# Optimization experiments

Measured on AMD Instinct MI355X. Metric: run time of the kernel, lower is better.

Reference implementation:

```python
import jax, jax.numpy as jnp
import numpy as np

POOL = 7
IMG = 1024.0
NUM_CLASSES = 2
R = 1000


def crop_and_resize(feat, boxes, pool):
    # feat: [C,H,W]; boxes: [N,4] normalized (y1,x1,y2,x2); returns [N,C,pool,pool]
    C, H, W = feat.shape
    y1, x1, y2, x2 = boxes[:, 0], boxes[:, 1], boxes[:, 2], boxes[:, 3]
    t = jnp.arange(pool, dtype=feat.dtype) / (pool - 1)
    ys = (y1[:, None] + (y2 - y1)[:, None] * t[None, :]) * (H - 1)  # [N,P]
    xs = (x1[:, None] + (x2 - x1)[:, None] * t[None, :]) * (W - 1)  # [N,P]
    vy = (ys >= 0) & (ys <= H - 1)
    vx = (xs >= 0) & (xs <= W - 1)
    yf = jnp.floor(ys)
    xf = jnp.floor(xs)
    wy = (ys - yf)[None, :, :, None]  # [1,N,P,1]
    wx = (xs - xf)[None, :, None, :]  # [1,N,1,P]
    y0 = jnp.clip(yf, 0, H - 1).astype(jnp.int32)
    y1i = jnp.clip(yf + 1, 0, H - 1).astype(jnp.int32)
    x0 = jnp.clip(xf, 0, W - 1).astype(jnp.int32)
    x1i = jnp.clip(xf + 1, 0, W - 1).astype(jnp.int32)

    def g(yi, xi):  # gather -> [C,N,P,P]
        return feat[:, yi[:, :, None], xi[:, None, :]]

    val = (g(y0, x0) * (1 - wy) * (1 - wx)
           + g(y0, x1i) * (1 - wy) * wx
           + g(y1i, x0) * wy * (1 - wx)
           + g(y1i, x1i) * wy * wx)
    mask = (vy[:, :, None] & vx[:, None, :])[None]  # extrapolation value 0
    return jnp.where(mask, val, 0.0).transpose(1, 0, 2, 3)


def roi_align(feats, rois_flat):
    # rois_flat: [N,4] in pixel coords (x1,y1,x2,y2)
    x1, y1, x2, y2 = rois_flat[:, 0], rois_flat[:, 1], rois_flat[:, 2], rois_flat[:, 3]
    lvl = jnp.log2(jnp.sqrt((y2 - y1) * (x2 - x1)) / 224.0)
    lvl = jnp.clip(jnp.round(lvl) + 4, 2, 5)
    boxes = rois_flat[:, jnp.array([1, 0, 3, 2])] / IMG  # (y1,x1,y2,x2) normalized
    crops = jnp.stack([crop_and_resize(f[0], boxes, POOL) for f in feats])  # [4,N,C,P,P]
    sel = (lvl[None, :] == jnp.arange(2, 6, dtype=lvl.dtype)[:, None])       # [4,N]
    return jnp.sum(jnp.where(sel[:, :, None, None, None], crops, 0.0), axis=0)  # [N,C,P,P]


def setup_inputs() -> dict:
    key = jax.random.key(0)
    ks = jax.random.split(key, 24)
    feat2 = jax.random.normal(ks[0], (1, 256, 256, 256), jnp.float32)
    feat3 = jax.random.normal(ks[1], (1, 256, 128, 128), jnp.float32)
    feat4 = jax.random.normal(ks[2], (1, 256, 64, 64), jnp.float32)
    feat5 = jax.random.normal(ks[3], (1, 256, 32, 32), jnp.float32)
    x1 = jax.random.uniform(ks[4], (1, R), minval=0.0, maxval=900.0)
    y1 = jax.random.uniform(ks[5], (1, R), minval=0.0, maxval=900.0)
    w = jax.random.uniform(ks[6], (1, R), minval=16.0, maxval=400.0)
    h = jax.random.uniform(ks[7], (1, R), minval=16.0, maxval=400.0)
    rois = jnp.stack([x1, y1, jnp.minimum(x1 + w, 1023.0), jnp.minimum(y1 + h, 1023.0)], axis=-1)
    s = 0.02
    params = dict(
        conv_w=s * jax.random.normal(ks[8], (1024, 256, POOL, POOL), jnp.float32),
        conv_b=jnp.zeros((1024,), jnp.float32),
        bn_gamma=jnp.ones((1024,), jnp.float32),
        bn_beta=jnp.zeros((1024,), jnp.float32),
        bn_mean=jnp.zeros((1024,), jnp.float32),
        bn_var=jnp.ones((1024,), jnp.float32),
        fc1_w=s * jax.random.normal(ks[9], (1024, 1024), jnp.float32),
        fc1_b=jnp.zeros((1024,), jnp.float32),
        fc2_w=s * jax.random.normal(ks[10], (1024, 1024), jnp.float32),
        fc2_b=jnp.zeros((1024,), jnp.float32),
        cls_w=s * jax.random.normal(ks[11], (NUM_CLASSES, 1024), jnp.float32),
        cls_b=jnp.zeros((NUM_CLASSES,), jnp.float32),
        bbox_w=s * jax.random.normal(ks[12], (NUM_CLASSES * 4, 1024), jnp.float32),
        bbox_b=jnp.zeros((NUM_CLASSES * 4,), jnp.float32),
    )
    return dict(feat2=feat2, feat3=feat3, feat4=feat4, feat5=feat5, rois=rois, **params)


def reference(feat2, feat3, feat4, feat5, rois, conv_w, conv_b, bn_gamma, bn_beta,
              bn_mean, bn_var, fc1_w, fc1_b, fc2_w, fc2_b, cls_w, cls_b, bbox_w, bbox_b):
    roi_number = rois.shape[1]
    pooled = roi_align([feat2, feat3, feat4, feat5], rois.reshape(-1, 4))  # [N,256,7,7]
    # conv1 (7x7 valid on 7x7 input -> 1x1 spatial) + BN (inference stats, eps=1e-3)
    y = jnp.einsum('nchw,ochw->no', pooled, conv_w) + conv_b
    y = (y - bn_mean) / jnp.sqrt(bn_var + 1e-3) * bn_gamma + bn_beta
    h = jax.nn.relu(y @ fc1_w.T + fc1_b)
    h = jax.nn.relu(h @ fc2_w.T + fc2_b)
    logits = h @ cls_w.T + cls_b
    probs = jax.nn.softmax(logits, axis=-1)
    bbox = h @ bbox_w.T + bbox_b
    return (logits.reshape(1, roi_number, NUM_CLASSES),
            probs.reshape(1, roi_number, NUM_CLASSES),
            bbox.reshape(1, roi_number, NUM_CLASSES, 4))
```

## Files before the change

kernel.cpp:

```cpp
#include <hip/hip_runtime.h>
#include <cstdint>
#include <cstddef>

typedef __attribute__((ext_vector_type(8))) short bf16x8;
typedef __attribute__((ext_vector_type(4))) float f32x4;

#define POOLK 12544

#define TOFF2 0
#define TOFF3 16777216
#define TOFF4 20971520
#define TOFF5 22020096
#define TTOT_SH 22282240

__device__ __forceinline__ void gld16(const void* g, void* l) {
    __builtin_amdgcn_global_load_lds(
        (const __attribute__((address_space(1))) void*)g,
        (__attribute__((address_space(3))) void*)l, 16, 0, 0);
}

__device__ __forceinline__ unsigned short f32_to_bf16(float f) {
    union { float f; unsigned u; } x; x.f = f;
    unsigned r = (x.u + 0x7FFFu + ((x.u >> 16) & 1u)) >> 16;
    return (unsigned short)r;
}
__device__ __forceinline__ float bf16_to_f32(unsigned short s) {
    return __uint_as_float(((unsigned)s) << 16);
}

__global__ __launch_bounds__(256) void feat_tr_kernel(
    const float* __restrict__ f2, const float* __restrict__ f3,
    const float* __restrict__ f4, const float* __restrict__ f5,
    unsigned short* __restrict__ T)
{
    int b = blockIdx.x;
    const float* src; unsigned short* dst; int P;
    if (b < 2048)      { src = f2; dst = T + TOFF2; P = 65536; }
    else if (b < 2560) { src = f3; dst = T + TOFF3; P = 16384; b -= 2048; }
    else if (b < 2688) { src = f4; dst = T + TOFF4; P = 4096;  b -= 2560; }
    else               { src = f5; dst = T + TOFF5; P = 1024;  b -= 2688; }
    const int p0 = b * 32;
    __shared__ float lds[32][260];
    const int t = threadIdx.x;
    const int cr = t >> 3, x4 = (t & 7) * 4;
#pragma unroll
    for (int cc = 0; cc < 8; ++cc) {
        const int c = cc * 32 + cr;
        const float4 v = *(const float4*)(src + (size_t)c * P + p0 + x4);
        lds[x4+0][c] = v.x; lds[x4+1][c] = v.y;
        lds[x4+2][c] = v.z; lds[x4+3][c] = v.w;
    }
    __syncthreads();
    const int c0 = (t & 31) * 8;
#pragma unroll
    for (int pz = 0; pz < 4; ++pz) {
        const int pp = pz * 8 + (t >> 5);
        const float4 a = *(const float4*)&lds[pp][c0];
        const float4 bq = *(const float4*)&lds[pp][c0 + 4];
        bf16x8 o;
        o[0] = (short)f32_to_bf16(a.x);  o[1] = (short)f32_to_bf16(a.y);
        o[2] = (short)f32_to_bf16(a.z);  o[3] = (short)f32_to_bf16(a.w);
        o[4] = (short)f32_to_bf16(bq.x); o[5] = (short)f32_to_bf16(bq.y);
        o[6] = (short)f32_to_bf16(bq.z); o[7] = (short)f32_to_bf16(bq.w);
        *(bf16x8*)(dst + ((size_t)(p0 + pp)) * 256 + c0) = o;
    }
}

__global__ __launch_bounds__(256) void roi_gather_kernel(
    const unsigned short* __restrict__ T, const float* __restrict__ rois,
    unsigned short* __restrict__ pooled)
{
    const int n = blockIdx.x;
    const int tid = threadIdx.x;
    __shared__ int sy0[7], sy1[7], sx0[7], sx1[7];
    __shared__ float swy[7], swx[7], svy[7], svx[7];

    const float rx1 = rois[n*4+0], ry1 = rois[n*4+1];
    const float rx2 = rois[n*4+2], ry2 = rois[n*4+3];
    int lvl = (int)rintf(log2f(sqrtf((ry2-ry1)*(rx2-rx1)) * (1.0f/224.0f))) + 4;
    lvl = lvl < 2 ? 2 : (lvl > 5 ? 5 : lvl);
    const int W = 256 >> (lvl - 2);
    const float Hm1 = (float)(W - 1);
    const unsigned short* Tl = T + (lvl == 2 ? TOFF2 : (lvl == 3 ? TOFF3 : (lvl == 4 ? TOFF4 : TOFF5)));

    if (tid < 7) {
        const float t = (float)tid / 6.0f;
        const float by1 = ry1*(1.0f/1024.0f), by2 = ry2*(1.0f/1024.0f);
        const float bx1 = rx1*(1.0f/1024.0f), bx2 = rx2*(1.0f/1024.0f);
        const float ys = (by1 + (by2 - by1) * t) * Hm1;
        const float xs = (bx1 + (bx2 - bx1) * t) * Hm1;
        const float yf = floorf(ys), xf = floorf(xs);
        swy[tid] = ys - yf;  swx[tid] = xs - xf;
        sy0[tid] = (int)fminf(fmaxf(yf,        0.0f), Hm1);
        sy1[tid] = (int)fminf(fmaxf(yf + 1.0f, 0.0f), Hm1);
        sx0[tid] = (int)fminf(fmaxf(xf,        0.0f), Hm1);
        sx1[tid] = (int)fminf(fmaxf(xf + 1.0f, 0.0f), Hm1);
        svy[tid] = (ys >= 0.0f && ys <= Hm1) ? 1.0f : 0.0f;
        svx[tid] = (xs >= 0.0f && xs <= Hm1) ? 1.0f : 0.0f;
    }
    __syncthreads();

    const int g  = tid >> 5;
    const int c0 = (tid & 31) * 8;
    unsigned short* orow = pooled + (size_t)n * POOLK;
#pragma unroll
    for (int it = 0; it < 7; ++it) {
        const int pos = it * 8 + g;
        if (pos >= 49) break;
        const int i = pos / 7, j = pos % 7;
        const int y0 = sy0[i], y1 = sy1[i], x0 = sx0[j], x1 = sx1[j];
        const float wy = swy[i], wx = swx[j];
        const float scale = svy[i] * svx[j];
        const bf16x8 v00 = *(const bf16x8*)(Tl + ((size_t)(y0*W + x0))*256 + c0);
        const bf16x8 v01 = *(const bf16x8*)(Tl + ((size_t)(y0*W + x1))*256 + c0);
        const bf16x8 v10 = *(const bf16x8*)(Tl + ((size_t)(y1*W + x0))*256 + c0);
        const bf16x8 v11 = *(const bf16x8*)(Tl + ((size_t)(y1*W + x1))*256 + c0);
        bf16x8 o;
#pragma unroll
        for (int jj = 0; jj < 8; ++jj) {
            const float f00 = bf16_to_f32((unsigned short)v00[jj]);
            const float f01 = bf16_to_f32((unsigned short)v01[jj]);
            const float f10 = bf16_to_f32((unsigned short)v10[jj]);
            const float f11 = bf16_to_f32((unsigned short)v11[jj]);
            const float top = f00 + (f01 - f00) * wx;
            const float bot = f10 + (f11 - f10) * wx;
            o[jj] = (short)f32_to_bf16((top + (bot - top) * wy) * scale);
        }
        *(bf16x8*)(orow + pos * 256 + c0) = o;
    }
}

__global__ __launch_bounds__(256) void roi_direct_kernel(
    const float* __restrict__ feat2, const float* __restrict__ feat3,
    const float* __restrict__ feat4, const float* __restrict__ feat5,
    const float* __restrict__ rois, unsigned short* __restrict__ pooled)
{
    const int n = blockIdx.x;
    const int tid = threadIdx.x;
    __shared__ int sy0[7], sy1[7], sx0[7], sx1[7];
    __shared__ float swy[7], swx[7], svy[7], svx[7];
    const float rx1 = rois[n*4+0], ry1 = rois[n*4+1];
    const float rx2 = rois[n*4+2], ry2 = rois[n*4+3];
    int lvl = (int)rintf(log2f(sqrtf((ry2-ry1)*(rx2-rx1)) * (1.0f/224.0f))) + 4;
    lvl = lvl < 2 ? 2 : (lvl > 5 ? 5 : lvl);
    const int H = 256 >> (lvl - 2);
    const float Hm1 = (float)(H - 1);
    const float* feat = lvl==2 ? feat2 : (lvl==3 ? feat3 : (lvl==4 ? feat4 : feat5));
    if (tid < 7) {
        const float t = (float)tid / 6.0f;
        const float by1 = ry1*(1.0f/1024.0f), by2 = ry2*(1.0f/1024.0f);
        const float bx1 = rx1*(1.0f/1024.0f), bx2 = rx2*(1.0f/1024.0f);
        const float ys = (by1 + (by2-by1)*t) * Hm1;
        const float xs = (bx1 + (bx2-bx1)*t) * Hm1;
        const float yf = floorf(ys), xf = floorf(xs);
        swy[tid] = ys - yf;  swx[tid] = xs - xf;
        sy0[tid] = (int)fminf(fmaxf(yf,      0.0f), Hm1);
        sy1[tid] = (int)fminf(fmaxf(yf+1.0f, 0.0f), Hm1);
        sx0[tid] = (int)fminf(fmaxf(xf,      0.0f), Hm1);
        sx1[tid] = (int)fminf(fmaxf(xf+1.0f, 0.0f), Hm1);
        svy[tid] = (ys >= 0.0f && ys <= Hm1) ? 1.0f : 0.0f;
        svx[tid] = (xs >= 0.0f && xs <= Hm1) ? 1.0f : 0.0f;
    }
    __syncthreads();
    const int HW = H * H;
    unsigned short* orow = pooled + (size_t)n * POOLK;
    for (int e = tid; e < POOLK; e += 256) {
        const int c = e / 49, ij = e % 49, i = ij / 7, j = ij % 7;
        const float* p = feat + c * HW;
        const int y0 = sy0[i], y1 = sy1[i], x0 = sx0[j], x1 = sx1[j];
        const float wy = swy[i], wx = swx[j];
        const float v00 = p[y0*H + x0], v01 = p[y0*H + x1];
        const float v10 = p[y1*H + x0], v11 = p[y1*H + x1];
        float v = v00*(1.0f-wy)*(1.0f-wx) + v01*(1.0f-wy)*wx
                + v10*wy*(1.0f-wx)        + v11*wy*wx;
        v *= svy[i] * svx[j];
        orow[ij*256 + c] = f32_to_bf16(v);
    }
}

__global__ void cvt_bf16_kernel(const float* __restrict__ src,
                                unsigned short* __restrict__ dst, int n)
{
    const int i = (blockIdx.x * 256 + threadIdx.x) * 4;
    if (i >= n) return;
    const float4 v = *(const float4*)(src + i);
    ushort4 o;
    o.x = f32_to_bf16(v.x); o.y = f32_to_bf16(v.y);
    o.z = f32_to_bf16(v.z); o.w = f32_to_bf16(v.w);
    *(ushort4*)(dst + i) = o;
}

__global__ __launch_bounds__(256) void convw_tr_kernel(
    const float* __restrict__ src, unsigned short* __restrict__ dst)
{
    const int o = blockIdx.x;
    const int t = threadIdx.x;
    __shared__ unsigned short wlds[POOLK];
    const float* srow = src + (size_t)o * POOLK;
    for (int it = 0; it < 49; ++it) {
        const int idx = it * 256 + t;
        wlds[idx] = f32_to_bf16(srow[idx]);
    }
    __syncthreads();
    unsigned short* drow = dst + (size_t)o * POOLK;
    for (int it = 0; it < 49; ++it) {
        const int k = it * 256 + t;
        const int c = k & 255, ij = k >> 8;
        drow[k] = wlds[c * 49 + ij];
    }
}

__global__ __launch_bounds__(256, 2) void gemm_bt(
    const unsigned short* __restrict__ A, const unsigned short* __restrict__ B,
    float* __restrict__ Cpart, int K, int Kper, int nz)
{
    __shared__ __align__(16) unsigned short At[128*64];
    __shared__ __align__(16) unsigned short Bt[128*64];
    const int tid  = threadIdx.x;
    const int lane = tid & 63;
    const int bid  = blockIdx.x;
    const int z  = bid % nz;
    const int iq = bid / nz;
    const int bx = iq & 7, by = iq >> 3;
    const int wm = (tid >> 6) >> 1, wn = (tid >> 6) & 1;
    const size_t k0 = (size_t)z * Kper;

    const int r1 = tid >> 3;
    const int q  = tid & 7;
    const int csw = (q ^ (r1 & 7)) * 8;
    const unsigned short* Ag = A + ((size_t)(by * 128 + r1)) * K + k0 + csw;
    const unsigned short* Bg = B + ((size_t)(bx * 128 + r1)) * K + k0 + csw;

    f32x4 acc[4][4] = {};
    const int fr = lane & 15;
    const int fq = lane >> 4;
    const int sA = fr & 7;

    for (int k = 0; k < Kper; k += 64) {
#pragma unroll
        for (int p = 0; p < 4; ++p) {
            gld16(Ag + (size_t)(32 * p) * K + k, &At[p * 2048 + tid * 8]);
            gld16(Bg + (size_t)(32 * p) * K + k, &Bt[p * 2048 + tid * 8]);
        }
        asm volatile("s_waitcnt vmcnt(0)" ::: "memory");
        __syncthreads();

        bf16x8 a[4][2], b[4][2];
#pragma unroll
        for (int mi = 0; mi < 4; ++mi) {
            const int row = wm * 64 + mi * 16 + fr;
#pragma unroll
            for (int kk = 0; kk < 2; ++kk)
                a[mi][kk] = *(const bf16x8*)&At[row * 64 + ((kk * 4 + fq) ^ sA) * 8];
        }
#pragma unroll
        for (int ni = 0; ni < 4; ++ni) {
            const int row = wn * 64 + ni * 16 + fr;
#pragma unroll
            for (int kk = 0; kk < 2; ++kk)
                b[ni][kk] = *(const bf16x8*)&Bt[row * 64 + ((kk * 4 + fq) ^ sA) * 8];
        }
#pragma unroll
        for (int mi = 0; mi < 4; ++mi)
#pragma unroll
            for (int ni = 0; ni < 4; ++ni)
                acc[mi][ni] = __builtin_amdgcn_mfma_f32_16x16x32_bf16(
                    a[mi][0], b[ni][0], acc[mi][ni], 0, 0, 0);
        if (k + 32 < Kper) {
#pragma unroll
            for (int mi = 0; mi < 4; ++mi)
#pragma unroll
                for (int ni = 0; ni < 4; ++ni)
                    acc[mi][ni] = __builtin_amdgcn_mfma_f32_16x16x32_bf16(
                        a[mi][1], b[ni][1], acc[mi][ni], 0, 0, 0);
        }
        __syncthreads();
    }

    float* Cp = Cpart + (size_t)z * (1024 * 1024);
    const int row0 = by * 128 + wm * 64;
    const int col0 = bx * 128 + wn * 64;
#pragma unroll
    for (int mi = 0; mi < 4; ++mi)
#pragma unroll
        for (int ni = 0; ni < 4; ++ni)
#pragma unroll
            for (int r = 0; r < 4; ++r)
                Cp[(size_t)(row0 + mi*16 + fq*4 + r) * 1024 + col0 + ni*16 + fr]
                    = acc[mi][ni][r];
}

__global__ void reduce_bn_kernel(const float* __restrict__ part,
    const float* __restrict__ bias, const float* __restrict__ gamma,
    const float* __restrict__ beta, const float* __restrict__ mean,
    const float* __restrict__ var, unsigned short* __restrict__ out, int nz)
{
    const int i4 = (blockIdx.x * 256 + threadIdx.x) * 4;
    const int n = i4 & 1023;
    float4 v = make_float4(0.f, 0.f, 0.f, 0.f);
    for (int zz = 0; zz < nz; ++zz) {
        const float4 p = *(const float4*)(part + (size_t)zz * 1048576 + i4);
        v.x += p.x; v.y += p.y; v.z += p.z; v.w += p.w;
    }
    const float4 bi = *(const float4*)(bias + n);
    const float4 ga = *(const float4*)(gamma + n);
    const float4 be = *(const float4*)(beta + n);
    const float4 me = *(const float4*)(mean + n);
    const float4 va = *(const float4*)(var + n);
    ushort4 o;
    o.x = f32_to_bf16((v.x + bi.x - me.x) * __frsqrt_rn(va.x + 0.001f) * ga.x + be.x);
    o.y = f32_to_bf16((v.y + bi.y - me.y) * __frsqrt_rn(va.y + 0.001f) * ga.y + be.y);
    o.z = f32_to_bf16((v.z + bi.z - me.z) * __frsqrt_rn(va.z + 0.001f) * ga.z + be.z);
    o.w = f32_to_bf16((v.w + bi.w - me.w) * __frsqrt_rn(va.w + 0.001f) * ga.w + be.w);
    *(ushort4*)(out + i4) = o;
}

__global__ __launch_bounds__(256) void gemm64_fused(
    const unsigned short* __restrict__ A, const unsigned short* __restrict__ B,
    const float* __restrict__ bias, unsigned short* __restrict__ out, int relu)
{
    __shared__ __align__(16) unsigned short At[64*64];
    __shared__ __align__(16) unsigned short Bt[64*64];
    const int tid = threadIdx.x, lane = tid & 63;
    const int w = tid >> 6, wm = w >> 1, wn = w & 1;
    const int r1 = tid >> 3;
    const int q  = tid & 7;
    const int csw = (q ^ (r1 & 7)) * 8;
    const unsigned short* Ag = A + (size_t)(blockIdx.y*64 + r1) * 1024 + csw;
    const unsigned short* Bg = B + (size_t)(blockIdx.x*64 + r1) * 1024 + csw;
    const int fr = lane & 15, fq = lane >> 4;
    const int sA = fr & 7;
    f32x4 acc[2][2] = {};
    for (int k = 0; k < 1024; k += 64) {
#pragma unroll
        for (int p = 0; p < 2; ++p) {
            gld16(Ag + (size_t)(32 * p) * 1024 + k, &At[p * 2048 + tid * 8]);
            gld16(Bg + (size_t)(32 * p) * 1024 + k, &Bt[p * 2048 + tid * 8]);
        }
        asm volatile("s_waitcnt vmcnt(0)" ::: "memory");
        __syncthreads();
        bf16x8 a[2][2], b[2][2];
#pragma unroll
        for (int mi = 0; mi < 2; ++mi) {
            const int row = wm * 32 + mi * 16 + fr;
#pragma unroll
            for (int kk = 0; kk < 2; ++kk)
                a[mi][kk] = *(const bf16x8*)&At[row * 64 + ((kk * 4 + fq) ^ sA) * 8];
        }
#pragma unroll
        for (int ni = 0; ni < 2; ++ni) {
            const int row = wn * 32 + ni * 16 + fr;
#pragma unroll
            for (int kk = 0; kk < 2; ++kk)
                b[ni][kk] = *(const bf16x8*)&Bt[row * 64 + ((kk * 4 + fq) ^ sA) * 8];
        }
#pragma unroll
        for (int kk = 0; kk < 2; ++kk)
#pragma unroll
            for (int mi = 0; mi < 2; ++mi)
#pragma unroll
                for (int ni = 0; ni < 2; ++ni)
                    acc[mi][ni] = __builtin_amdgcn_mfma_f32_16x16x32_bf16(
                        a[mi][kk], b[ni][kk], acc[mi][ni], 0, 0, 0);
        __syncthreads();
    }
    const int row0 = blockIdx.y*64 + wm*32;
    const int col0 = blockIdx.x*64 + wn*32;
#pragma unroll
    for (int mi = 0; mi < 2; ++mi)
#pragma unroll
        for (int ni = 0; ni < 2; ++ni)
#pragma unroll
            for (int r = 0; r < 4; ++r) {
                const int row = row0 + mi*16 + fq*4 + r;
                const int col = col0 + ni*16 + fr;
                float v = acc[mi][ni][r] + bias[col];
                if (relu) v = fmaxf(v, 0.0f);
                out[(size_t)row * 1024 + col] = f32_to_bf16(v);
            }
}

__global__ __launch_bounds__(256) void head_kernel(
    const unsigned short* __restrict__ h2,
    const float* __restrict__ cls_w, const float* __restrict__ cls_b,
    const float* __restrict__ bbox_w, const float* __restrict__ bbox_b,
    float* __restrict__ out)
{
    const int roi = blockIdx.x * 4 + (threadIdx.x >> 6);
    const int lane = threadIdx.x & 63;
    const unsigned short* hrow = h2 + (size_t)roi * 1024;
    float hv[16];
#pragma unroll
    for (int j = 0; j < 16; ++j)
        hv[j] = bf16_to_f32(hrow[lane*16 + j]);
    float r[10];
#pragma unroll
    for (int o = 0; o < 10; ++o) {
        const float* w = (o < 2) ? (cls_w + o*1024) : (bbox_w + (size_t)(o-2)*1024);
        float s = 0.f;
#pragma unroll
        for (int j = 0; j < 16; ++j) s += hv[j] * w[lane*16 + j];
#pragma unroll
        for (int off = 32; off > 0; off >>= 1) s += __shfl_xor(s, off);
        r[o] = s;
    }
    if (lane == 0) {
        const float l0 = r[0] + cls_b[0], l1 = r[1] + cls_b[1];
        out[roi*2+0] = l0; out[roi*2+1] = l1;
        const float m = fmaxf(l0, l1);
        const float e0 = expf(l0 - m), e1 = expf(l1 - m);
        const float inv = 1.0f / (e0 + e1);
        out[2000 + roi*2 + 0] = e0 * inv;
        out[2000 + roi*2 + 1] = e1 * inv;
#pragma unroll
        for (int qq = 0; qq < 8; ++qq) out[4000 + roi*8 + qq] = r[2+qq] + bbox_b[qq];
    }
}

extern "C" void kernel_launch(void* const* d_in, const int* in_sizes, int n_in,
                              void* d_out, int out_size, void* d_ws, size_t ws_size,
                              hipStream_t stream)
{
    const float* feat2   = (const float*)d_in[0];
    const float* feat3   = (const float*)d_in[1];
    const float* feat4   = (const float*)d_in[2];
    const float* feat5   = (const float*)d_in[3];
    const float* rois    = (const float*)d_in[4];
    const float* conv_w  = (const float*)d_in[5];
    const float* conv_b  = (const float*)d_in[6];
    const float* bn_gamma= (const float*)d_in[7];
    const float* bn_beta = (const float*)d_in[8];
    const float* bn_mean = (const float*)d_in[9];
    const float* bn_var  = (const float*)d_in[10];
    const float* fc1_w   = (const float*)d_in[11];
    const float* fc1_b   = (const float*)d_in[12];
    const float* fc2_w   = (const float*)d_in[13];
    const float* fc2_b   = (const float*)d_in[14];
    const float* cls_w   = (const float*)d_in[15];
    const float* cls_b   = (const float*)d_in[16];
    const float* bbox_w  = (const float*)d_in[17];
    const float* bbox_b  = (const float*)d_in[18];
    float* out = (float*)d_out;

    const size_t fixedBytes = (size_t)25690112 + 25690112 + 5 * (size_t)2097152;
    const size_t needA = fixedBytes + (size_t)44564480;
    const size_t needB = fixedBytes + (size_t)16777216;
    int tier = (ws_size >= needA) ? 1 : 2;
    (void)needB;
    const size_t regionA = tier == 1 ? (size_t)44564480 : (size_t)16777216;
    const int nzc  = tier == 1 ? 8 : 4;
    const int Kper = tier == 1 ? 1568 : 3136;

    char* ws = (char*)d_ws;
    size_t off = 0;
    auto alloc = [&](size_t bytes) {
        void* p = ws + off; off += (bytes + 255) & ~(size_t)255; return p;
    };
    char* rA = (char*)alloc(regionA);
    unsigned short* T    = (unsigned short*)rA;
    float*          part = (float*)rA;
    unsigned short* pooled   = (unsigned short*)alloc((size_t)1024 * POOLK * 2);
    unsigned short* convw_bf = (unsigned short*)alloc((size_t)1024 * POOLK * 2);
    unsigned short* fc1w_bf  = (unsigned short*)alloc((size_t)1048576 * 2);
    unsigned short* fc2w_bf  = (unsigned short*)alloc((size_t)1048576 * 2);
    unsigned short* ybf      = (unsigned short*)alloc((size_t)1048576 * 2);
    unsigned short* h1bf     = (unsigned short*)alloc((size_t)1048576 * 2);
    unsigned short* h2bf     = (unsigned short*)alloc((size_t)1048576 * 2);

    hipLaunchKernelGGL(cvt_bf16_kernel, dim3(1024), dim3(256), 0, stream,
                       fc1_w, fc1w_bf, 1048576);
    hipLaunchKernelGGL(cvt_bf16_kernel, dim3(1024), dim3(256), 0, stream,
                       fc2_w, fc2w_bf, 1048576);
    hipLaunchKernelGGL(convw_tr_kernel, dim3(1024), dim3(256), 0, stream,
                       conv_w, convw_bf);

    hipMemsetAsync(pooled + (size_t)1000 * POOLK, 0, (size_t)24 * POOLK * 2, stream);

    if (tier == 1) {
        hipLaunchKernelGGL(feat_tr_kernel, dim3(2720), dim3(256), 0, stream,
                           feat2, feat3, feat4, feat5, T);
        hipLaunchKernelGGL(roi_gather_kernel, dim3(1000), dim3(256), 0, stream,
                           T, rois, pooled);
    } else {
        hipLaunchKernelGGL(roi_direct_kernel, dim3(1000), dim3(256), 0, stream,
                           feat2, feat3, feat4, feat5, rois, pooled);
    }

    hipLaunchKernelGGL(gemm_bt, dim3(64 * nzc), dim3(256), 0, stream,
                       pooled, convw_bf, part, POOLK, Kper, nzc);
    hipLaunchKernelGGL(reduce_bn_kernel, dim3(1024), dim3(256), 0, stream,
                       part, conv_b, bn_gamma, bn_beta, bn_mean, bn_var, ybf, nzc);

    hipLaunchKernelGGL(gemm64_fused, dim3(16, 16), dim3(256), 0, stream,
                       ybf, fc1w_bf, fc1_b, h1bf, 1);
    hipLaunchKernelGGL(gemm64_fused, dim3(16, 16), dim3(256), 0, stream,
                       h1bf, fc2w_bf, fc2_b, h2bf, 1);

    hipLaunchKernelGGL(head_kernel, dim3(250), dim3(256), 0, stream,
                       h2bf, cls_w, cls_b, bbox_w, bbox_b, out);
}
```

Baseline: 132.7 us.

## Fuse prep kernels, fold padding memset into ROI gather, double-buffer GEMM K loops

Merges feature transpose, conv weight transpose and FC weight conversion into one prep launch, now with bf16 LDS staging and XOR swizzle. The padding-row memset moves into the ROI gather kernel. Both GEMMs switch from a single 64-wide K tile to double-buffered 32-wide K tiles that prefetch the next tile while MFMAs run, and raise wave priority around the MFMAs. The goal is fewer launches and less load latency exposed in the GEMM loops, at the cost of more barriers per K step.

```diff
diff --git a/kernel.cpp b/kernel.cpp
--- a/kernel.cpp
+++ b/kernel.cpp
@@ -11,67 +11,103 @@
 #define TOFF3 16777216
 #define TOFF4 20971520
 #define TOFF5 22020096
-#define TTOT_SH 22282240
 
 __device__ __forceinline__ void gld16(const void* g, void* l) {
     __builtin_amdgcn_global_load_lds(
         (const __attribute__((address_space(1))) void*)g,
         (__attribute__((address_space(3))) void*)l, 16, 0, 0);
 }
-
 __device__ __forceinline__ unsigned short f32_to_bf16(float f) {
     union { float f; unsigned u; } x; x.f = f;
-    unsigned r = (x.u + 0x7FFFu + ((x.u >> 16) & 1u)) >> 16;
-    return (unsigned short)r;
+    return (unsigned short)((x.u + 0x7FFFu + ((x.u >> 16) & 1u)) >> 16);
 }
 __device__ __forceinline__ float bf16_to_f32(unsigned short s) {
     return __uint_as_float(((unsigned)s) << 16);
 }
 
-__global__ __launch_bounds__(256) void feat_tr_kernel(
+__global__ __launch_bounds__(256) void prep_kernel(
     const float* __restrict__ f2, const float* __restrict__ f3,
     const float* __restrict__ f4, const float* __restrict__ f5,
-    unsigned short* __restrict__ T)
-{
+    unsigned short* __restrict__ T,
+    const float* __restrict__ conv_w, unsigned short* __restrict__ convw_bf,
+    const float* __restrict__ fc1_w, unsigned short* __restrict__ fc1w_bf,
+    const float* __restrict__ fc2_w, unsigned short* __restrict__ fc2w_bf,
+    int do_feat)
+{
+    __shared__ __align__(16) unsigned short sh[8192];
+    const int t = threadIdx.x;
     int b = blockIdx.x;
-    const float* src; unsigned short* dst; int P;
-    if (b < 2048)      { src = f2; dst = T + TOFF2; P = 65536; }
-    else if (b < 2560) { src = f3; dst = T + TOFF3; P = 16384; b -= 2048; }
-    else if (b < 2688) { src = f4; dst = T + TOFF4; P = 4096;  b -= 2560; }
-    else               { src = f5; dst = T + TOFF5; P = 1024;  b -= 2688; }
-    const int p0 = b * 32;
-    __shared__ float lds[32][260];
-    const int t = threadIdx.x;
-    const int cr = t >> 3, x4 = (t & 7) * 4;
-#pragma unroll
-    for (int cc = 0; cc < 8; ++cc) {
-        const int c = cc * 32 + cr;
-        const float4 v = *(const float4*)(src + (size_t)c * P + p0 + x4);
-        lds[x4+0][c] = v.x; lds[x4+1][c] = v.y;
-        lds[x4+2][c] = v.z; lds[x4+3][c] = v.w;
-    }
-    __syncthreads();
-    const int c0 = (t & 31) * 8;
-#pragma unroll
-    for (int pz = 0; pz < 4; ++pz) {
-        const int pp = pz * 8 + (t >> 5);
-        const float4 a = *(const float4*)&lds[pp][c0];
-        const float4 bq = *(const float4*)&lds[pp][c0 + 4];
-        bf16x8 o;
-        o[0] = (short)f32_to_bf16(a.x);  o[1] = (short)f32_to_bf16(a.y);
-        o[2] = (short)f32_to_bf16(a.z);  o[3] = (short)f32_to_bf16(a.w);
-        o[4] = (short)f32_to_bf16(bq.x); o[5] = (short)f32_to_bf16(bq.y);
-        o[6] = (short)f32_to_bf16(bq.z); o[7] = (short)f32_to_bf16(bq.w);
-        *(bf16x8*)(dst + ((size_t)(p0 + pp)) * 256 + c0) = o;
+
+    if (b < 2720) {
+        if (!do_feat) return;
+        const float* src; unsigned short* dst; int P;
+        if (b < 2048)      { src = f2; dst = T + TOFF2; P = 65536; }
+        else if (b < 2560) { src = f3; dst = T + TOFF3; P = 16384; b -= 2048; }
+        else if (b < 2688) { src = f4; dst = T + TOFF4; P = 4096;  b -= 2560; }
+        else               { src = f5; dst = T + TOFF5; P = 1024;  b -= 2688; }
+        const int p0 = b * 32;
+        const int cr = t >> 3, x4 = (t & 7) * 4;
+#pragma unroll
+        for (int cc = 0; cc < 8; ++cc) {
+            const int c = cc * 32 + cr;
+            const float4 v = *(const float4*)(src + (size_t)c * P + p0 + x4);
+            const int blk = c >> 3, cl = c & 7;
+            float vv[4] = {v.x, v.y, v.z, v.w};
+#pragma unroll
+            for (int i = 0; i < 4; ++i) {
+                const int p = x4 + i;
+                sh[p * 256 + ((blk ^ (p >> 2)) << 3) + cl] = f32_to_bf16(vv[i]);
+            }
+        }
+        __syncthreads();
+        const int cb = t & 31;
+#pragma unroll
+        for (int pz = 0; pz < 4; ++pz) {
+            const int pp = pz * 8 + (t >> 5);
+            const bf16x8 v = *(const bf16x8*)&sh[pp * 256 + ((cb ^ (pp >> 2)) << 3)];
+            *(bf16x8*)(dst + (size_t)(p0 + pp) * 256 + cb * 8) = v;
+        }
+        return;
+    }
+    b -= 2720;
+    if (b < 2048) {
+        const int o = b >> 1, half = b & 1;
+        const float* srow = conv_w + (size_t)o * POOLK + half * 6272;
+        for (int k = t; k < 6272; k += 256) sh[k] = f32_to_bf16(srow[k]);
+        __syncthreads();
+        unsigned short* drow = convw_bf + (size_t)o * POOLK + half * 128;
+        for (int k = t; k < 6272; k += 256) {
+            const int ij = k >> 7, cl = k & 127;
+            drow[ij * 256 + cl] = sh[cl * 49 + ij];
+        }
+        return;
+    }
+    b -= 2048;
+    {
+        const float* src = (b < 1024) ? fc1_w : fc2_w;
+        unsigned short* dst = (b < 1024) ? fc1w_bf : fc2w_bf;
+        const int bb = b & 1023;
+        const int i = (bb * 256 + t) * 4;
+        const float4 v = *(const float4*)(src + i);
+        ushort4 o;
+        o.x = f32_to_bf16(v.x); o.y = f32_to_bf16(v.y);
+        o.z = f32_to_bf16(v.z); o.w = f32_to_bf16(v.w);
+        *(ushort4*)(dst + i) = o;
     }
 }
 
 __global__ __launch_bounds__(256) void roi_gather_kernel(
     const unsigned short* __restrict__ T, const float* __restrict__ rois,
-    unsigned short* __restrict__ pooled)
+    unsigned short* __restrict__ pooled, int nroi)
 {
     const int n = blockIdx.x;
     const int tid = threadIdx.x;
+    unsigned short* orow = pooled + (size_t)n * POOLK;
+    if (n >= nroi) {
+        const bf16x8 z = {};
+        for (int k = tid * 8; k < POOLK; k += 2048) *(bf16x8*)(orow + k) = z;
+        return;
+    }
     __shared__ int sy0[7], sy1[7], sx0[7], sx1[7];
     __shared__ float swy[7], swx[7], svy[7], svx[7];
 
@@ -102,7 +138,6 @@
 
     const int g  = tid >> 5;
     const int c0 = (tid & 31) * 8;
-    unsigned short* orow = pooled + (size_t)n * POOLK;
 #pragma unroll
     for (int it = 0; it < 7; ++it) {
         const int pos = it * 8 + g;
@@ -133,10 +168,16 @@
 __global__ __launch_bounds__(256) void roi_direct_kernel(
     const float* __restrict__ feat2, const float* __restrict__ feat3,
     const float* __restrict__ feat4, const float* __restrict__ feat5,
-    const float* __restrict__ rois, unsigned short* __restrict__ pooled)
+    const float* __restrict__ rois, unsigned short* __restrict__ pooled, int nroi)
 {
     const int n = blockIdx.x;
     const int tid = threadIdx.x;
+    unsigned short* orow = pooled + (size_t)n * POOLK;
+    if (n >= nroi) {
+        const bf16x8 z = {};
+        for (int k = tid * 8; k < POOLK; k += 2048) *(bf16x8*)(orow + k) = z;
+        return;
+    }
     __shared__ int sy0[7], sy1[7], sx0[7], sx1[7];
     __shared__ float swy[7], swx[7], svy[7], svx[7];
     const float rx1 = rois[n*4+0], ry1 = rois[n*4+1];
@@ -163,7 +204,6 @@
     }
     __syncthreads();
     const int HW = H * H;
-    unsigned short* orow = pooled + (size_t)n * POOLK;
     for (int e = tid; e < POOLK; e += 256) {
         const int c = e / 49, ij = e % 49, i = ij / 7, j = ij % 7;
         const float* p = feat + c * HW;
@@ -178,44 +218,12 @@
     }
 }
 
-__global__ void cvt_bf16_kernel(const float* __restrict__ src,
-                                unsigned short* __restrict__ dst, int n)
-{
-    const int i = (blockIdx.x * 256 + threadIdx.x) * 4;
-    if (i >= n) return;
-    const float4 v = *(const float4*)(src + i);
-    ushort4 o;
-    o.x = f32_to_bf16(v.x); o.y = f32_to_bf16(v.y);
-    o.z = f32_to_bf16(v.z); o.w = f32_to_bf16(v.w);
-    *(ushort4*)(dst + i) = o;
-}
-
-__global__ __launch_bounds__(256) void convw_tr_kernel(
-    const float* __restrict__ src, unsigned short* __restrict__ dst)
-{
-    const int o = blockIdx.x;
-    const int t = threadIdx.x;
-    __shared__ unsigned short wlds[POOLK];
-    const float* srow = src + (size_t)o * POOLK;
-    for (int it = 0; it < 49; ++it) {
-        const int idx = it * 256 + t;
-        wlds[idx] = f32_to_bf16(srow[idx]);
-    }
-    __syncthreads();
-    unsigned short* drow = dst + (size_t)o * POOLK;
-    for (int it = 0; it < 49; ++it) {
-        const int k = it * 256 + t;
-        const int c = k & 255, ij = k >> 8;
-        drow[k] = wlds[c * 49 + ij];
-    }
-}
-
 __global__ __launch_bounds__(256, 2) void gemm_bt(
     const unsigned short* __restrict__ A, const unsigned short* __restrict__ B,
     float* __restrict__ Cpart, int K, int Kper, int nz)
 {
-    __shared__ __align__(16) unsigned short At[128*64];
-    __shared__ __align__(16) unsigned short Bt[128*64];
+    __shared__ __align__(16) unsigned short At[2][128*32];
+    __shared__ __align__(16) unsigned short Bt[2][128*32];
     const int tid  = threadIdx.x;
     const int lane = tid & 63;
     const int bid  = blockIdx.x;
@@ -225,56 +233,54 @@
     const int wm = (tid >> 6) >> 1, wn = (tid >> 6) & 1;
     const size_t k0 = (size_t)z * Kper;
 
-    const int r1 = tid >> 3;
-    const int q  = tid & 7;
-    const int csw = (q ^ (r1 & 7)) * 8;
+    const int r1 = tid >> 2;
+    const int q  = tid & 3;
+    const int csw = (q ^ (r1 & 3)) * 8;
     const unsigned short* Ag = A + ((size_t)(by * 128 + r1)) * K + k0 + csw;
     const unsigned short* Bg = B + ((size_t)(bx * 128 + r1)) * K + k0 + csw;
+    const int nit = Kper >> 5;
+
+    gld16(Ag,                  &At[0][tid * 8]);
+    gld16(Ag + (size_t)64 * K, &At[0][(tid + 256) * 8]);
+    gld16(Bg,                  &Bt[0][tid * 8]);
+    gld16(Bg + (size_t)64 * K, &Bt[0][(tid + 256) * 8]);
 
     f32x4 acc[4][4] = {};
     const int fr = lane & 15;
     const int fq = lane >> 4;
-    const int sA = fr & 7;
-
-    for (int k = 0; k < Kper; k += 64) {
-#pragma unroll
-        for (int p = 0; p < 4; ++p) {
-            gld16(Ag + (size_t)(32 * p) * K + k, &At[p * 2048 + tid * 8]);
-            gld16(Bg + (size_t)(32 * p) * K + k, &Bt[p * 2048 + tid * 8]);
+    const int rslot = (fq ^ (fr & 3)) * 8;
+
+    int buf = 0;
+    for (int it = 0; it < nit; ++it) {
+        if (it + 1 < nit) {
+            const size_t ko = (size_t)(it + 1) * 32;
+            gld16(Ag + ko,                  &At[buf ^ 1][tid * 8]);
+            gld16(Ag + (size_t)64 * K + ko, &At[buf ^ 1][(tid + 256) * 8]);
+            gld16(Bg + ko,                  &Bt[buf ^ 1][tid * 8]);
+            gld16(Bg + (size_t)64 * K + ko, &Bt[buf ^ 1][(tid + 256) * 8]);
+            asm volatile("s_waitcnt vmcnt(4)" ::: "memory");
+        } else {
+            asm volatile("s_waitcnt vmcnt(0)" ::: "memory");
         }
-        asm volatile("s_waitcnt vmcnt(0)" ::: "memory");
         __syncthreads();
 
-        bf16x8 a[4][2], b[4][2];
-#pragma unroll
-        for (int mi = 0; mi < 4; ++mi) {
-            const int row = wm * 64 + mi * 16 + fr;
-#pragma unroll
-            for (int kk = 0; kk < 2; ++kk)
-                a[mi][kk] = *(const bf16x8*)&At[row * 64 + ((kk * 4 + fq) ^ sA) * 8];
-        }
-#pragma unroll
-        for (int ni = 0; ni < 4; ++ni) {
-            const int row = wn * 64 + ni * 16 + fr;
-#pragma unroll
-            for (int kk = 0; kk < 2; ++kk)
-                b[ni][kk] = *(const bf16x8*)&Bt[row * 64 + ((kk * 4 + fq) ^ sA) * 8];
-        }
+        bf16x8 a[4], b[4];
+#pragma unroll
+        for (int mi = 0; mi < 4; ++mi)
+            a[mi] = *(const bf16x8*)&At[buf][(wm*64 + mi*16 + fr) * 32 + rslot];
+#pragma unroll
+        for (int ni = 0; ni < 4; ++ni)
+            b[ni] = *(const bf16x8*)&Bt[buf][(wn*64 + ni*16 + fr) * 32 + rslot];
+        __builtin_amdgcn_s_setprio(1);
 #pragma unroll
         for (int mi = 0; mi < 4; ++mi)
 #pragma unroll
             for (int ni = 0; ni < 4; ++ni)
                 acc[mi][ni] = __builtin_amdgcn_mfma_f32_16x16x32_bf16(
-                    a[mi][0], b[ni][0], acc[mi][ni], 0, 0, 0);
-        if (k + 32 < Kper) {
-#pragma unroll
-            for (int mi = 0; mi < 4; ++mi)
-#pragma unroll
-                for (int ni = 0; ni < 4; ++ni)
-                    acc[mi][ni] = __builtin_amdgcn_mfma_f32_16x16x32_bf16(
-                        a[mi][1], b[ni][1], acc[mi][ni], 0, 0, 0);
-        }
+                    a[mi], b[ni], acc[mi][ni], 0, 0, 0);
+        __builtin_amdgcn_s_setprio(0);
         __syncthreads();
+        buf ^= 1;
     }
 
     float* Cp = Cpart + (size_t)z * (1024 * 1024);
@@ -319,50 +325,50 @@
     const unsigned short* __restrict__ A, const unsigned short* __restrict__ B,
     const float* __restrict__ bias, unsigned short* __restrict__ out, int relu)
 {
-    __shared__ __align__(16) unsigned short At[64*64];
-    __shared__ __align__(16) unsigned short Bt[64*64];
+    __shared__ __align__(16) unsigned short At[2][64*32];
+    __shared__ __align__(16) unsigned short Bt[2][64*32];
     const int tid = threadIdx.x, lane = tid & 63;
     const int w = tid >> 6, wm = w >> 1, wn = w & 1;
-    const int r1 = tid >> 3;
-    const int q  = tid & 7;
-    const int csw = (q ^ (r1 & 7)) * 8;
+    const int r1 = tid >> 2;
+    const int q  = tid & 3;
+    const int csw = (q ^ (r1 & 3)) * 8;
     const unsigned short* Ag = A + (size_t)(blockIdx.y*64 + r1) * 1024 + csw;
     const unsigned short* Bg = B + (size_t)(blockIdx.x*64 + r1) * 1024 + csw;
     const int fr = lane & 15, fq = lane >> 4;
-    const int sA = fr & 7;
+    const int rslot = (fq ^ (fr & 3)) * 8;
+
+    gld16(Ag, &At[0][tid * 8]);
+    gld16(Bg, &Bt[0][tid * 8]);
+
     f32x4 acc[2][2] = {};
-    for (int k = 0; k < 1024; k += 64) {
-#pragma unroll
-        for (int p = 0; p < 2; ++p) {
-            gld16(Ag + (size_t)(32 * p) * 1024 + k, &At[p * 2048 + tid * 8]);
-            gld16(Bg + (size_t)(32 * p) * 1024 + k, &Bt[p * 2048 + tid * 8]);
+    int buf = 0;
+    for (int it = 0; it < 32; ++it) {
+        if (it + 1 < 32) {
+            const int ko = (it + 1) * 32;
+            gld16(Ag + ko, &At[buf ^ 1][tid * 8]);
+            gld16(Bg + ko, &Bt[buf ^ 1][tid * 8]);
+            asm volatile("s_waitcnt vmcnt(2)" ::: "memory");
+        } else {
+            asm volatile("s_waitcnt vmcnt(0)" ::: "memory");
         }
-        asm volatile("s_waitcnt vmcnt(0)" ::: "memory");
         __syncthreads();
-        bf16x8 a[2][2], b[2][2];
-#pragma unroll
-        for (int mi = 0; mi < 2; ++mi) {
-            const int row = wm * 32 + mi * 16 + fr;
-#pragma unroll
-            for (int kk = 0; kk < 2; ++kk)
-                a[mi][kk] = *(const bf16x8*)&At[row * 64 + ((kk * 4 + fq) ^ sA) * 8];
-        }
-#pragma unroll
-        for (int ni = 0; ni < 2; ++ni) {
-            const int row = wn * 32 + ni * 16 + fr;
-#pragma unroll
-            for (int kk = 0; kk < 2; ++kk)
-                b[ni][kk] = *(const bf16x8*)&Bt[row * 64 + ((kk * 4 + fq) ^ sA) * 8];
-        }
-#pragma unroll
-        for (int kk = 0; kk < 2; ++kk)
-#pragma unroll
-            for (int mi = 0; mi < 2; ++mi)
-#pragma unroll
-                for (int ni = 0; ni < 2; ++ni)
-                    acc[mi][ni] = __builtin_amdgcn_mfma_f32_16x16x32_bf16(
-                        a[mi][kk], b[ni][kk], acc[mi][ni], 0, 0, 0);
+        bf16x8 a[2], b[2];
+#pragma unroll
+        for (int mi = 0; mi < 2; ++mi)
+            a[mi] = *(const bf16x8*)&At[buf][(wm*32 + mi*16 + fr) * 32 + rslot];
+#pragma unroll
+        for (int ni = 0; ni < 2; ++ni)
+            b[ni] = *(const bf16x8*)&Bt[buf][(wn*32 + ni*16 + fr) * 32 + rslot];
+        __builtin_amdgcn_s_setprio(1);
+#pragma unroll
+        for (int mi = 0; mi < 2; ++mi)
+#pragma unroll
+            for (int ni = 0; ni < 2; ++ni)
+                acc[mi][ni] = __builtin_amdgcn_mfma_f32_16x16x32_bf16(
+                    a[mi], b[ni], acc[mi][ni], 0, 0, 0);
+        __builtin_amdgcn_s_setprio(0);
         __syncthreads();
+        buf ^= 1;
     }
     const int row0 = blockIdx.y*64 + wm*32;
     const int col0 = blockIdx.x*64 + wn*32;
@@ -441,12 +447,11 @@
     const float* bbox_w  = (const float*)d_in[17];
     const float* bbox_b  = (const float*)d_in[18];
     float* out = (float*)d_out;
+    const int nroi = in_sizes[4] / 4;
 
     const size_t fixedBytes = (size_t)25690112 + 25690112 + 5 * (size_t)2097152;
     const size_t needA = fixedBytes + (size_t)44564480;
-    const size_t needB = fixedBytes + (size_t)16777216;
-    int tier = (ws_size >= needA) ? 1 : 2;
-    (void)needB;
+    const int tier = (ws_size >= needA) ? 1 : 2;
     const size_t regionA = tier == 1 ? (size_t)44564480 : (size_t)16777216;
     const int nzc  = tier == 1 ? 8 : 4;
     const int Kper = tier == 1 ? 1568 : 3136;
@@ -467,23 +472,17 @@
     unsigned short* h1bf     = (unsigned short*)alloc((size_t)1048576 * 2);
     unsigned short* h2bf     = (unsigned short*)alloc((size_t)1048576 * 2);
 
-    hipLaunchKernelGGL(cvt_bf16_kernel, dim3(1024), dim3(256), 0, stream,
-                       fc1_w, fc1w_bf, 1048576);
-    hipLaunchKernelGGL(cvt_bf16_kernel, dim3(1024), dim3(256), 0, stream,
-                       fc2_w, fc2w_bf, 1048576);
-    hipLaunchKernelGGL(convw_tr_kernel, dim3(1024), dim3(256), 0, stream,
-                       conv_w, convw_bf);
-
-    hipMemsetAsync(pooled + (size_t)1000 * POOLK, 0, (size_t)24 * POOLK * 2, stream);
+    hipLaunchKernelGGL(prep_kernel, dim3(6816), dim3(256), 0, stream,
+                       feat2, feat3, feat4, feat5, T,
+                       conv_w, convw_bf, fc1_w, fc1w_bf, fc2_w, fc2w_bf,
+                       tier == 1 ? 1 : 0);
 
     if (tier == 1) {
-        hipLaunchKernelGGL(feat_tr_kernel, dim3(2720), dim3(256), 0, stream,
-                           feat2, feat3, feat4, feat5, T);
-        hipLaunchKernelGGL(roi_gather_kernel, dim3(1000), dim3(256), 0, stream,
-                           T, rois, pooled);
+        hipLaunchKernelGGL(roi_gather_kernel, dim3(1024), dim3(256), 0, stream,
+                           T, rois, pooled, nroi);
     } else {
-        hipLaunchKernelGGL(roi_direct_kernel, dim3(1000), dim3(256), 0, stream,
-                           feat2, feat3, feat4, feat5, rois, pooled);
+        hipLaunchKernelGGL(roi_direct_kernel, dim3(1024), dim3(256), 0, stream,
+                           feat2, feat3, feat4, feat5, rois, pooled, nroi);
     }
 
     hipLaunchKernelGGL(gemm_bt, dim3(64 * nzc), dim3(256), 0, stream,
```

Result: faster. 128.1 us (-3.5%).
